# Kernel optimization log

Hardware: AMD Instinct MI355X
Metric: run time of the kernel (lower is better)

## Reference

```python
import jax, jax.numpy as jnp
import numpy as np
import math

N_HEADS = 16
D_MODEL = 1024
D_K = D_MODEL // N_HEADS
B, T = 16, 512


def setup_inputs() -> dict:
    key = jax.random.key(0)
    ks = jax.random.split(key, 8)
    x = jax.random.normal(ks[0], (B, T, D_MODEL), dtype=jnp.float32)
    mask = jnp.ones((B, 1, T), dtype=bool)
    pos = jax.random.normal(ks[1], (1, 2 * T - 1, D_MODEL), dtype=jnp.float32)
    s = 1.0 / math.sqrt(D_MODEL)
    qvk_w = jax.random.normal(ks[2], (D_MODEL, 3 * D_MODEL), dtype=jnp.float32) * s
    qvk_b = jnp.zeros((3 * D_MODEL,), dtype=jnp.float32)
    pos_w = jax.random.normal(ks[3], (D_MODEL, D_MODEL), dtype=jnp.float32) * s
    # xavier_normal on [1,1,nh,d_k]
    pstd = math.sqrt(2.0 / (N_HEADS + D_K))
    posu = jax.random.normal(ks[4], (1, 1, N_HEADS, D_K), dtype=jnp.float32) * pstd
    posv = jax.random.normal(ks[5], (1, 1, N_HEADS, D_K), dtype=jnp.float32) * pstd
    return {"x": x, "mask": mask, "pos": pos, "qvk_w": qvk_w, "qvk_b": qvk_b,
            "pos_w": pos_w, "posu": posu, "posv": posv}


def _shift(matrix_bd):
    # matrix_bd: [b, nh, t, 2t-1] -> gather relative positions -> [b, nh, t, t]
    b, nh, t, _ = matrix_bd.shape
    r = jnp.arange(t)
    rel_pos = (r[None, :] - r[:, None]) + (t - 1)          # [t, t]
    idx = rel_pos[None, None]                               # [1,1,t,t]
    return jnp.take_along_axis(matrix_bd, jnp.broadcast_to(idx, (b, nh, t, t)), axis=3)


def reference(x, mask, pos, qvk_w, qvk_b, pos_w, posu, posv):
    b, t, d = x.shape
    nh, dk = N_HEADS, D_K
    h = x @ qvk_w + qvk_b                                   # [b, t, 3d]
    q, k, v = jnp.split(h, 3, axis=-1)
    q = q.reshape(b, t, nh, dk)                             # [b, t, nh, dk]
    k = k.reshape(b, t, nh, dk).transpose(0, 2, 1, 3)       # [b, nh, t, dk]
    v = v.reshape(b, t, nh, dk).transpose(0, 2, 1, 3)
    p = (pos @ pos_w).reshape(pos.shape[0], -1, nh, dk).transpose(0, 2, 1, 3)  # [1, nh, 2t-1, dk]
    qu = (q + posu).transpose(0, 2, 1, 3)                   # [b, nh, t, dk]
    qv = (q + posv).transpose(0, 2, 1, 3)
    matrix_ac = jnp.einsum('bhtd,bhsd->bhts', qu, k)        # [b, nh, t, t]
    matrix_bd = jnp.einsum('bhtd,hpd->bhtp', qv, p[0])      # [b, nh, t, 2t-1]
    matrix_bd = _shift(matrix_bd)                           # [b, nh, t, t]
    scores = (matrix_ac + matrix_bd) / math.sqrt(dk)
    m = mask[:, None]                                       # [b, 1, 1, t]
    scores = jnp.where(m, scores, -jnp.inf)
    weights = jax.nn.softmax(scores, axis=-1)
    context = jnp.einsum('bhts,bhsd->bhtd', weights, v)     # [b, nh, t, dk]
    context = context.transpose(0, 2, 1, 3).reshape(b, t, nh * dk)
    # enable_output_proj is falsy (dropout_rate=0.0 passed into that slot) -> no output proj
    return context, weights
```

## Files before the change

kernel.cpp:

```cpp
#include <hip/hip_runtime.h>

typedef _Float16 f16;
typedef _Float16 half8 __attribute__((ext_vector_type(8)));
typedef float floatx4 __attribute__((ext_vector_type(4)));

#define MFMA16(a, b, c) __builtin_amdgcn_mfma_f32_16x16x32_f16(a, b, c, 0, 0, 0)

typedef const __attribute__((address_space(1))) unsigned int* gas_t;
typedef __attribute__((address_space(3))) unsigned int* las_t;
__device__ __forceinline__ void gload16(const void* g, void* l) {
    __builtin_amdgcn_global_load_lds((gas_t)g, (las_t)l, 16, 0, 0);
}


__global__ void k_cvt(const float* __restrict__ in, f16* __restrict__ out, int n4) {
    int i = blockIdx.x * blockDim.x + threadIdx.x;
    if (i >= n4) return;
    float4 v = ((const float4*)in)[i];
    struct alignas(8) H4 { f16 a, b, c, d; };
    H4 o{(f16)v.x, (f16)v.y, (f16)v.z, (f16)v.w};
    ((H4*)out)[i] = o;
}

__global__ void k_cvt_pad(const float* __restrict__ in, f16* __restrict__ out, int n4, int n_in) {
    int i = blockIdx.x * blockDim.x + threadIdx.x;
    if (i >= n4) return;
    struct alignas(8) H4 { f16 a, b, c, d; };
    H4 o;
    if (i * 4 < n_in) {
        float4 v = ((const float4*)in)[i];
        o = H4{(f16)v.x, (f16)v.y, (f16)v.z, (f16)v.w};
    } else {
        o = H4{(f16)0.f, (f16)0.f, (f16)0.f, (f16)0.f};
    }
    ((H4*)out)[i] = o;
}

__global__ void k_transpose(const float* __restrict__ in, f16* __restrict__ out, int R, int C) {
    __shared__ float tile[32][33];
    int c0 = blockIdx.x * 32, r0 = blockIdx.y * 32;
    int tx = threadIdx.x & 31, ty = threadIdx.x >> 5;
#pragma unroll
    for (int i = 0; i < 32; i += 8)
        tile[ty + i][tx] = in[(size_t)(r0 + ty + i) * C + c0 + tx];
    __syncthreads();
#pragma unroll
    for (int i = 0; i < 32; i += 8)
        out[(size_t)(c0 + ty + i) * R + r0 + tx] = (f16)tile[tx][ty + i];
}


__device__ __forceinline__ void gemm_core(const f16* __restrict__ A, const f16* __restrict__ Bt,
                                          int K, int m0, int n0, f16* As, f16* Bs,
                                          floatx4 (&acc)[4][4]) {
    const int tid = threadIdx.x;
    const int lane = tid & 63, wave = tid >> 6;
    const int jj = lane & 15, g = lane >> 4;
    const int wm = (wave >> 1) * 64, wn = (wave & 1) * 64;
    const int gp = g ^ ((jj >> 1) & 3);

#pragma unroll
    for (int mt = 0; mt < 4; mt++)
#pragma unroll
        for (int nt = 0; nt < 4; nt++) acc[mt][nt] = floatx4{0.f, 0.f, 0.f, 0.f};

    const int p0 = tid, p1 = 256 + tid;
    const int r0 = p0 >> 2, k0 = (p0 & 3) ^ ((p0 >> 3) & 3);
    const int r1 = p1 >> 2, k1 = (p1 & 3) ^ ((p1 >> 3) & 3);
    const f16* ga0 = A + (size_t)(m0 + r0) * K + k0 * 8;
    const f16* ga1 = A + (size_t)(m0 + r1) * K + k1 * 8;
    const f16* gb0 = Bt + (size_t)(n0 + r0) * K + k0 * 8;
    const f16* gb1 = Bt + (size_t)(n0 + r1) * K + k1 * 8;
    f16* lA0 = As + (wave * 64) * 8;
    f16* lA1 = As + (256 + wave * 64) * 8;
    f16* lB0 = Bs + (wave * 64) * 8;
    f16* lB1 = Bs + (256 + wave * 64) * 8;

    const int iters = K >> 5;
    for (int kt = 0; kt < iters; ++kt) {
        const int ko = kt * 32;
        gload16(ga0 + ko, lA0);
        gload16(ga1 + ko, lA1);
        gload16(gb0 + ko, lB0);
        gload16(gb1 + ko, lB1);
        __syncthreads();
        half8 af[4], bf[4];
#pragma unroll
        for (int mt = 0; mt < 4; mt++)
            af[mt] = ((const half8*)As)[(wm + mt * 16 + jj) * 4 + gp];
#pragma unroll
        for (int nt = 0; nt < 4; nt++)
            bf[nt] = ((const half8*)Bs)[(wn + nt * 16 + jj) * 4 + gp];
#pragma unroll
        for (int mt = 0; mt < 4; mt++)
#pragma unroll
            for (int nt = 0; nt < 4; nt++)
                acc[mt][nt] = MFMA16(af[mt], bf[nt], acc[mt][nt]);
        __syncthreads();
    }
}

__global__ __launch_bounds__(256) void k_gemm_qkv(const f16* __restrict__ xA, const f16* __restrict__ wT,
                                                  const float* __restrict__ bias,
                                                  const float* __restrict__ pu, const float* __restrict__ pv,
                                                  f16* __restrict__ QU, f16* __restrict__ QV,
                                                  f16* __restrict__ Kb, f16* __restrict__ VT) {
    __shared__ __align__(16) f16 smem[16704];
    f16* As = smem;
    f16* Bs = smem + 4096;
    floatx4 acc[4][4];
    int m0 = blockIdx.y * 128, n0 = blockIdx.x * 128;
    gemm_core(xA, wT, 1024, m0, n0, As, Bs, acc);

    int tid = threadIdx.x;
    int lane = tid & 63, wave = tid >> 6;
    int jj = lane & 15, g = lane >> 4;
    int wm = (wave >> 1) * 64, wn = (wave & 1) * 64;
    int sect = n0 >> 10;

    if (sect == 2) {
        __syncthreads();
        f16* tb = smem;
#pragma unroll
        for (int nt = 0; nt < 4; nt++) {
            int col = wn + nt * 16 + jj;
            float bsv = bias[n0 + col];
#pragma unroll
            for (int mt = 0; mt < 4; mt++)
#pragma unroll
                for (int r = 0; r < 4; r++) {
                    int row = wm + mt * 16 + g * 4 + r;
                    tb[col * 130 + row] = (f16)(acc[mt][nt][r] + bsv);
                }
        }
        __syncthreads();
        int col = tid >> 1, hh = tid & 1;
        int C = n0 + col, head = (C & 1023) >> 6, dk = C & 63;
        int R = m0 + hh * 64, b = R >> 9, tt = R & 511;
        int bh = b * 16 + head;
        f16* dst = VT + ((size_t)bh * 64 + dk) * 512 + tt;
        const f16* srcp = tb + col * 130 + hh * 64;
#pragma unroll
        for (int i = 0; i < 8; i++)
            *(uint4*)(dst + i * 8) = *(const uint4*)(srcp + i * 8);
        return;
    }

#pragma unroll
    for (int nt = 0; nt < 4; nt++) {
        int C = n0 + wn + nt * 16 + jj;
        int cc = C & 1023, head = cc >> 6, dk = cc & 63;
        float bsv = bias[C];
        float uu = pu[cc], vv = pv[cc];
#pragma unroll
        for (int mt = 0; mt < 4; mt++) {
#pragma unroll
            for (int r = 0; r < 4; r++) {
                int R = m0 + wm + mt * 16 + g * 4 + r;
                int b = R >> 9, tt = R & 511;
                int bh = b * 16 + head;
                float val = acc[mt][nt][r] + bsv;
                if (sect == 0) {
                    QU[((size_t)bh * 512 + tt) * 64 + dk] = (f16)(val + uu);
                    QV[((size_t)bh * 512 + tt) * 64 + dk] = (f16)(val + vv);
                } else {
                    Kb[((size_t)bh * 512 + tt) * 64 + dk] = (f16)val;
                }
            }
        }
    }
}

__global__ __launch_bounds__(256) void k_gemm_p(const f16* __restrict__ posA, const f16* __restrict__ pwT,
                                                f16* __restrict__ P) {
    __shared__ __align__(16) f16 As[4096];
    __shared__ __align__(16) f16 Bs[4096];
    floatx4 acc[4][4];
    int m0 = blockIdx.y * 128, n0 = blockIdx.x * 128;
    gemm_core(posA, pwT, 1024, m0, n0, As, Bs, acc);

    int lane = threadIdx.x & 63, wave = threadIdx.x >> 6;
    int jj = lane & 15, g = lane >> 4;
    int wm = (wave >> 1) * 64, wn = (wave & 1) * 64;
#pragma unroll
    for (int nt = 0; nt < 4; nt++) {
        int C = n0 + wn + nt * 16 + jj;
        int head = C >> 6, dk = C & 63;
#pragma unroll
        for (int mt = 0; mt < 4; mt++) {
#pragma unroll
            for (int r = 0; r < 4; r++) {
                int R = m0 + wm + mt * 16 + g * 4 + r;
                float val = (R < 1023) ? acc[mt][nt][r] : 0.0f;
                P[((size_t)head * 1024 + R) * 64 + dk] = (f16)val;
            }
        }
    }
}

__global__ __launch_bounds__(256) void k_attn(const f16* __restrict__ QU, const f16* __restrict__ QV,
                                              const f16* __restrict__ Kb, const f16* __restrict__ VT,
                                              const f16* __restrict__ P,
                                              float* __restrict__ outc, float* __restrict__ outw) {
    __shared__ __align__(16) f16 wbuf[4][16][264];
    int lane = threadIdx.x & 63, wave = threadIdx.x >> 6;
    int bh = blockIdx.x >> 3, rb = blockIdx.x & 7;
    int b = bh >> 4, h = bh & 15;
    int R0 = rb * 64 + wave * 16;
    int jj = lane & 15, g = lane >> 4;

    const f16* qub = QU + ((size_t)bh * 512 + R0) * 64;
    const f16* qvb = QV + ((size_t)bh * 512 + R0) * 64;
    const f16* kb = Kb + (size_t)bh * 512 * 64;
    const f16* vtb = VT + (size_t)bh * 64 * 512;
    const f16* pb = P + (size_t)h * 1024 * 64;

    half8 qu0 = *(const half8*)(qub + jj * 64 + g * 8);
    half8 qu1 = *(const half8*)(qub + jj * 64 + 32 + g * 8);
    half8 qv0 = *(const half8*)(qvb + jj * 64 + g * 8);
    half8 qv1 = *(const half8*)(qvb + jj * 64 + 32 + g * 8);

    floatx4 S[32];
#pragma unroll
    for (int f = 0; f < 32; f++) S[f] = floatx4{0.f, 0.f, 0.f, 0.f};

#pragma unroll
    for (int jt = 0; jt < 32; jt++) {
        half8 b0 = *(const half8*)(kb + (jt * 16 + jj) * 64 + g * 8);
        half8 b1 = *(const half8*)(kb + (jt * 16 + jj) * 64 + 32 + g * 8);
        S[jt] = MFMA16(qu0, b0, S[jt]);
        S[jt] = MFMA16(qu1, b1, S[jt]);
    }

    int U0 = 496 - R0;
    int sl[4];
    bool cond[4];
#pragma unroll
    for (int r = 0; r < 4; r++) {
        int ii = g * 4 + r;
        sl[r] = (lane & 48) | ((jj + 15 - ii) & 15);
        cond[r] = (jj <= ii);
    }
#pragma unroll
    for (int t = 0; t < 33; t++) {
        const f16* prow = pb + (U0 + t * 16 + jj) * 64;
        half8 p0 = *(const half8*)(prow + g * 8);
        half8 p1 = *(const half8*)(prow + 32 + g * 8);
        floatx4 raw = floatx4{0.f, 0.f, 0.f, 0.f};
        raw = MFMA16(qv0, p0, raw);
        raw = MFMA16(qv1, p1, raw);
#pragma unroll
        for (int r = 0; r < 4; r++) {
            float rv = __shfl(raw[r], sl[r], 64);
            float lowv = cond[r] ? rv : 0.0f;
            float hiv = cond[r] ? 0.0f : rv;
            if (t < 32) S[t][r] += lowv;
            if (t > 0) S[t - 1][r] += hiv;
        }
    }

    float mx[4], inv[4];
#pragma unroll
    for (int r = 0; r < 4; r++) {
        float m = -1e30f;
#pragma unroll
        for (int f = 0; f < 32; f++) m = fmaxf(m, S[f][r]);
        m = fmaxf(m, __shfl_xor(m, 1, 64));
        m = fmaxf(m, __shfl_xor(m, 2, 64));
        m = fmaxf(m, __shfl_xor(m, 4, 64));
        m = fmaxf(m, __shfl_xor(m, 8, 64));
        mx[r] = m;
    }
#pragma unroll
    for (int f = 0; f < 32; f++)
#pragma unroll
        for (int r = 0; r < 4; r++) S[f][r] = __expf((S[f][r] - mx[r]) * 0.125f);
#pragma unroll
    for (int r = 0; r < 4; r++) {
        float s = 0.f;
#pragma unroll
        for (int f = 0; f < 32; f++) s += S[f][r];
        s += __shfl_xor(s, 1, 64);
        s += __shfl_xor(s, 2, 64);
        s += __shfl_xor(s, 4, 64);
        s += __shfl_xor(s, 8, 64);
        inv[r] = 1.0f / s;
    }

    floatx4 ctx[4];
#pragma unroll
    for (int nt = 0; nt < 4; nt++) ctx[nt] = floatx4{0.f, 0.f, 0.f, 0.f};
    float* wrow = outw + ((size_t)bh * 512 + R0) * 512;
#pragma unroll
    for (int half_ = 0; half_ < 2; half_++) {
#pragma unroll
        for (int f = 0; f < 16; f++) {
            int fg = half_ * 16 + f;
#pragma unroll
            for (int r = 0; r < 4; r++) {
                float wv = S[fg][r] * inv[r];
                int ii = g * 4 + r;
                __builtin_nontemporal_store(wv, &wrow[(size_t)ii * 512 + fg * 16 + jj]);
                wbuf[wave][ii][f * 16 + jj] = (f16)wv;
            }
        }
#pragma unroll
        for (int kk = 0; kk < 8; kk++) {
            half8 af = *(const half8*)(&wbuf[wave][0][0] + jj * 264 + kk * 32 + g * 8);
#pragma unroll
            for (int nt = 0; nt < 4; nt++) {
                half8 bf = *(const half8*)(vtb + (nt * 16 + jj) * 512 + half_ * 256 + kk * 32 + g * 8);
                ctx[nt] = MFMA16(af, bf, ctx[nt]);
            }
        }
    }
    float* crow = outc + ((size_t)b * 512 + R0) * 1024 + h * 64;
#pragma unroll
    for (int nt = 0; nt < 4; nt++)
#pragma unroll
        for (int r = 0; r < 4; r++)
            __builtin_nontemporal_store(ctx[nt][r], &crow[(size_t)(g * 4 + r) * 1024 + nt * 16 + jj]);
}


extern "C" void kernel_launch(void* const* d_in, const int* in_sizes, int n_in,
                              void* d_out, int out_size, void* d_ws, size_t ws_size,
                              hipStream_t stream) {
    const float* x = (const float*)d_in[0];
    const float* pos = (const float*)d_in[2];
    const float* qvk_w = (const float*)d_in[3];
    const float* qvk_b = (const float*)d_in[4];
    const float* pos_w = (const float*)d_in[5];
    const float* pu = (const float*)d_in[6];
    const float* pv = (const float*)d_in[7];

    float* outc = (float*)d_out;
    float* outw = outc + (size_t)16 * 512 * 1024;

    char* ws = (char*)d_ws;
    f16* xA = (f16*)(ws);
    f16* wT = (f16*)(ws + 16777216);
    f16* posA = (f16*)(ws + 23068672);
    f16* pwT = (f16*)(ws + 25165824);
    f16* QU = (f16*)(ws + 27262976);
    f16* QV = (f16*)(ws + 44040192);
    f16* Kb = (f16*)(ws + 60817408);
    f16* VT = (f16*)(ws + 77594624);
    f16* Pp = (f16*)(ws + 94371840);

    k_cvt<<<8192, 256, 0, stream>>>(x, xA, 2097152);
    k_cvt_pad<<<1024, 256, 0, stream>>>(pos, posA, 262144, 1047552);
    k_transpose<<<dim3(96, 32), 256, 0, stream>>>(qvk_w, wT, 1024, 3072);
    k_transpose<<<dim3(32, 32), 256, 0, stream>>>(pos_w, pwT, 1024, 1024);

    k_gemm_qkv<<<dim3(24, 64), 256, 0, stream>>>(xA, wT, qvk_b, pu, pv, QU, QV, Kb, VT);
    k_gemm_p<<<dim3(8, 8), 256, 0, stream>>>(posA, pwT, Pp);

    k_attn<<<2048, 256, 0, stream>>>(QU, QV, Kb, VT, Pp, outc, outw);
}
```

Baseline: 641.6 us.

## Split attention key dimension across two waves with cross-wave softmax reduction

```diff
diff --git a/kernel.cpp b/kernel.cpp
--- a/kernel.cpp
+++ b/kernel.cpp
@@ -198,20 +198,24 @@
     }
 }
 
-__global__ __launch_bounds__(256) void k_attn(const f16* __restrict__ QU, const f16* __restrict__ QV,
-                                              const f16* __restrict__ Kb, const f16* __restrict__ VT,
-                                              const f16* __restrict__ P,
-                                              float* __restrict__ outc, float* __restrict__ outw) {
-    __shared__ __align__(16) f16 wbuf[4][16][264];
-    int lane = threadIdx.x & 63, wave = threadIdx.x >> 6;
-    int bh = blockIdx.x >> 3, rb = blockIdx.x & 7;
+__global__ __launch_bounds__(128, 3) void k_attn(const f16* __restrict__ QU, const f16* __restrict__ QV,
+                                                 const f16* __restrict__ Kb, const f16* __restrict__ VT,
+                                                 const f16* __restrict__ P,
+                                                 float* __restrict__ outc, float* __restrict__ outw) {
+    __shared__ __align__(16) f16 wbuf[2][16][264];
+    __shared__ float redmax[2][16];
+    __shared__ float redsum[2][16];
+    __shared__ __align__(16) float cbuf[64][20];
+    int lane = threadIdx.x & 63;
+    int q = threadIdx.x >> 6;
+    int bh = blockIdx.x >> 5, rb = blockIdx.x & 31;
     int b = bh >> 4, h = bh & 15;
-    int R0 = rb * 64 + wave * 16;
+    int R0 = rb * 16;
     int jj = lane & 15, g = lane >> 4;
 
     const f16* qub = QU + ((size_t)bh * 512 + R0) * 64;
     const f16* qvb = QV + ((size_t)bh * 512 + R0) * 64;
-    const f16* kb = Kb + (size_t)bh * 512 * 64;
+    const f16* kb = Kb + ((size_t)bh * 512 + q * 256) * 64;
     const f16* vtb = VT + (size_t)bh * 64 * 512;
     const f16* pb = P + (size_t)h * 1024 * 64;
 
@@ -220,19 +224,19 @@
     half8 qv0 = *(const half8*)(qvb + jj * 64 + g * 8);
     half8 qv1 = *(const half8*)(qvb + jj * 64 + 32 + g * 8);
 
-    floatx4 S[32];
-#pragma unroll
-    for (int f = 0; f < 32; f++) S[f] = floatx4{0.f, 0.f, 0.f, 0.f};
-
-#pragma unroll
-    for (int jt = 0; jt < 32; jt++) {
+    floatx4 S[16];
+#pragma unroll
+    for (int f = 0; f < 16; f++) S[f] = floatx4{0.f, 0.f, 0.f, 0.f};
+
+#pragma unroll
+    for (int jt = 0; jt < 16; jt++) {
         half8 b0 = *(const half8*)(kb + (jt * 16 + jj) * 64 + g * 8);
         half8 b1 = *(const half8*)(kb + (jt * 16 + jj) * 64 + 32 + g * 8);
         S[jt] = MFMA16(qu0, b0, S[jt]);
         S[jt] = MFMA16(qu1, b1, S[jt]);
     }
 
-    int U0 = 496 - R0;
+    int U0 = 496 - R0 + q * 256;
     int sl[4];
     bool cond[4];
 #pragma unroll
@@ -242,7 +246,7 @@
         cond[r] = (jj <= ii);
     }
 #pragma unroll
-    for (int t = 0; t < 33; t++) {
+    for (int t = 0; t < 17; t++) {
         const f16* prow = pb + (U0 + t * 16 + jj) * 64;
         half8 p0 = *(const half8*)(prow + g * 8);
         half8 p1 = *(const half8*)(prow + 32 + g * 8);
@@ -254,72 +258,87 @@
             float rv = __shfl(raw[r], sl[r], 64);
             float lowv = cond[r] ? rv : 0.0f;
             float hiv = cond[r] ? 0.0f : rv;
-            if (t < 32) S[t][r] += lowv;
+            if (t < 16) S[t][r] += lowv;
             if (t > 0) S[t - 1][r] += hiv;
         }
     }
 
-    float mx[4], inv[4];
+    float mx[4], sm[4], inv[4];
 #pragma unroll
     for (int r = 0; r < 4; r++) {
         float m = -1e30f;
 #pragma unroll
-        for (int f = 0; f < 32; f++) m = fmaxf(m, S[f][r]);
+        for (int f = 0; f < 16; f++) m = fmaxf(m, S[f][r]);
         m = fmaxf(m, __shfl_xor(m, 1, 64));
         m = fmaxf(m, __shfl_xor(m, 2, 64));
         m = fmaxf(m, __shfl_xor(m, 4, 64));
         m = fmaxf(m, __shfl_xor(m, 8, 64));
         mx[r] = m;
-    }
-#pragma unroll
-    for (int f = 0; f < 32; f++)
+        if (jj == 0) redmax[q][g * 4 + r] = m;
+    }
+    __syncthreads();
+#pragma unroll
+    for (int r = 0; r < 4; r++) mx[r] = fmaxf(mx[r], redmax[q ^ 1][g * 4 + r]);
+#pragma unroll
+    for (int f = 0; f < 16; f++)
 #pragma unroll
         for (int r = 0; r < 4; r++) S[f][r] = __expf((S[f][r] - mx[r]) * 0.125f);
 #pragma unroll
     for (int r = 0; r < 4; r++) {
         float s = 0.f;
 #pragma unroll
-        for (int f = 0; f < 32; f++) s += S[f][r];
+        for (int f = 0; f < 16; f++) s += S[f][r];
         s += __shfl_xor(s, 1, 64);
         s += __shfl_xor(s, 2, 64);
         s += __shfl_xor(s, 4, 64);
         s += __shfl_xor(s, 8, 64);
-        inv[r] = 1.0f / s;
-    }
+        sm[r] = s;
+        if (jj == 0) redsum[q][g * 4 + r] = s;
+    }
+    __syncthreads();
+#pragma unroll
+    for (int r = 0; r < 4; r++) inv[r] = 1.0f / (sm[r] + redsum[q ^ 1][g * 4 + r]);
 
     floatx4 ctx[4];
 #pragma unroll
     for (int nt = 0; nt < 4; nt++) ctx[nt] = floatx4{0.f, 0.f, 0.f, 0.f};
-    float* wrow = outw + ((size_t)bh * 512 + R0) * 512;
-#pragma unroll
-    for (int half_ = 0; half_ < 2; half_++) {
-#pragma unroll
-        for (int f = 0; f < 16; f++) {
-            int fg = half_ * 16 + f;
-#pragma unroll
-            for (int r = 0; r < 4; r++) {
-                float wv = S[fg][r] * inv[r];
-                int ii = g * 4 + r;
-                __builtin_nontemporal_store(wv, &wrow[(size_t)ii * 512 + fg * 16 + jj]);
-                wbuf[wave][ii][f * 16 + jj] = (f16)wv;
-            }
-        }
-#pragma unroll
-        for (int kk = 0; kk < 8; kk++) {
-            half8 af = *(const half8*)(&wbuf[wave][0][0] + jj * 264 + kk * 32 + g * 8);
-#pragma unroll
-            for (int nt = 0; nt < 4; nt++) {
-                half8 bf = *(const half8*)(vtb + (nt * 16 + jj) * 512 + half_ * 256 + kk * 32 + g * 8);
-                ctx[nt] = MFMA16(af, bf, ctx[nt]);
-            }
-        }
-    }
-    float* crow = outc + ((size_t)b * 512 + R0) * 1024 + h * 64;
-#pragma unroll
-    for (int nt = 0; nt < 4; nt++)
-#pragma unroll
-        for (int r = 0; r < 4; r++)
-            __builtin_nontemporal_store(ctx[nt][r], &crow[(size_t)(g * 4 + r) * 1024 + nt * 16 + jj]);
+    float* wrow = outw + ((size_t)bh * 512 + R0) * 512 + q * 256;
+#pragma unroll
+    for (int f = 0; f < 16; f++) {
+#pragma unroll
+        for (int r = 0; r < 4; r++) {
+            float wv = S[f][r] * inv[r];
+            int ii = g * 4 + r;
+            __builtin_nontemporal_store(wv, &wrow[(size_t)ii * 512 + f * 16 + jj]);
+            wbuf[q][ii][f * 16 + jj] = (f16)wv;
+        }
+    }
+#pragma unroll
+    for (int kk = 0; kk < 8; kk++) {
+        half8 af = *(const half8*)(&wbuf[q][0][0] + jj * 264 + kk * 32 + g * 8);
+#pragma unroll
+        for (int nt = 0; nt < 4; nt++) {
+            half8 bf = *(const half8*)(vtb + (nt * 16 + jj) * 512 + q * 256 + kk * 32 + g * 8);
+            ctx[nt] = MFMA16(af, bf, ctx[nt]);
+        }
+    }
+
+    if (q == 1) {
+#pragma unroll
+        for (int nt = 0; nt < 4; nt++)
+            *(floatx4*)(&cbuf[lane][nt * 4]) = ctx[nt];
+    }
+    __syncthreads();
+    if (q == 0) {
+        float* crow = outc + ((size_t)b * 512 + R0) * 1024 + h * 64;
+#pragma unroll
+        for (int nt = 0; nt < 4; nt++) {
+            floatx4 o = ctx[nt] + *(const floatx4*)(&cbuf[lane][nt * 4]);
+#pragma unroll
+            for (int r = 0; r < 4; r++)
+                __builtin_nontemporal_store(o[r], &crow[(size_t)(g * 4 + r) * 1024 + nt * 16 + jj]);
+        }
+    }
 }
 
 
@@ -356,5 +375,5 @@
     k_gemm_qkv<<<dim3(24, 64), 256, 0, stream>>>(xA, wT, qvk_b, pu, pv, QU, QV, Kb, VT);
     k_gemm_p<<<dim3(8, 8), 256, 0, stream>>>(posA, pwT, Pp);
 
-    k_attn<<<2048, 256, 0, stream>>>(QU, QV, Kb, VT, Pp, outc, outw);
-}
+    k_attn<<<8192, 128, 0, stream>>>(QU, QV, Kb, VT, Pp, outc, outw);
+}
```

New measurement: 612.7 us. 4.5% less time.
